# Optimization experiments

Measured on AMD Instinct MI355X. Metric: run time of the kernel, lower is better.

Reference implementation:

```python
import jax, jax.numpy as jnp
import numpy as np

N, IN_SZ, OUT_SZ = 8192, 512, 64

def setup_inputs() -> dict:
    key = jax.random.key(0)
    ks = jax.random.split(key, 7)
    s_in = 1.0 / np.sqrt(IN_SZ)
    inp = {
        "input": jax.random.normal(ks[0], (N, IN_SZ), dtype=jnp.float32),
        "Wq": jax.random.uniform(ks[1], (OUT_SZ, IN_SZ), jnp.float32, -s_in, s_in),
        "bq": jax.random.uniform(ks[2], (OUT_SZ,), jnp.float32, -s_in, s_in),
        "Wk": jax.random.uniform(ks[3], (OUT_SZ, IN_SZ), jnp.float32, -s_in, s_in),
        "bk": jax.random.uniform(ks[4], (OUT_SZ,), jnp.float32, -s_in, s_in),
        "Wv": jax.random.uniform(ks[5], (OUT_SZ, IN_SZ), jnp.float32, -s_in, s_in),
        "bv": jax.random.uniform(ks[6], (OUT_SZ,), jnp.float32, -s_in, s_in),
    }
    return inp

def reference(input, Wq, bq, Wk, bk, Wv, bv):
    # torch nn.Linear: x @ W.T + b
    q = input @ Wq.T + bq  # [N, out]
    k = input @ Wk.T + bk  # [N, out]
    v = input @ Wv.T + bv  # [N, out]
    # NOTE: original module has NO 1/sqrt(d) scaling.
    scores = jax.nn.softmax(q @ k.T, axis=-1)  # [N, N]
    return scores @ v  # [N, out]
```

## Files before the change

kernel.cpp:

```cpp
#include <hip/hip_runtime.h>
#include <math.h>

#define SA_N   8192
#define SA_IN  512
#define SA_D   64
#define G_SPL  16

typedef short s16x8 __attribute__((ext_vector_type(8)));
typedef float f32x16 __attribute__((ext_vector_type(16)));

#define MFMA32(A, B, C) __builtin_amdgcn_mfma_f32_32x32x16_bf16((A), (B), (C), 0, 0, 0)

static __device__ __forceinline__ unsigned short f2bf_rn(float x) {
    unsigned int u = __float_as_uint(x);
    unsigned int r = (u + 0x7FFFu + ((u >> 16) & 1u)) >> 16;
    return (unsigned short)r;
}

static __device__ __forceinline__ void trunc_split(float f, unsigned short* hi, unsigned short* lo) {
    unsigned int u = __float_as_uint(f);
    *hi = (unsigned short)(u >> 16);
    float lf = f - __uint_as_float(u & 0xFFFF0000u);
    *lo = (unsigned short)(__float_as_uint(lf) >> 16);
}

static __device__ __forceinline__ void split8(const float4 a, const float4 b, s16x8* xh, s16x8* xl) {
    union { unsigned int u[4]; s16x8 v; } H, L;
    const float f[8] = {a.x, a.y, a.z, a.w, b.x, b.y, b.z, b.w};
#pragma unroll
    for (int p = 0; p < 4; ++p) {
        const unsigned int u0 = __float_as_uint(f[2 * p]);
        const unsigned int u1 = __float_as_uint(f[2 * p + 1]);
        H.u[p] = (u0 >> 16) | (u1 & 0xFFFF0000u);
        const float l0 = f[2 * p]     - __uint_as_float(u0 & 0xFFFF0000u);
        const float l1 = f[2 * p + 1] - __uint_as_float(u1 & 0xFFFF0000u);
        L.u[p] = (__float_as_uint(l0) >> 16) | (__float_as_uint(l1) & 0xFFFF0000u);
    }
    *xh = H.v; *xl = L.v;
}

static __device__ __forceinline__ s16x8 pack_rn8(const float4 a, const float4 b) {
    union { unsigned int u[4]; s16x8 v; } P;
    const float f[8] = {a.x, a.y, a.z, a.w, b.x, b.y, b.z, b.w};
#pragma unroll
    for (int p = 0; p < 4; ++p)
        P.u[p] = (unsigned int)f2bf_rn(f[2 * p]) | ((unsigned int)f2bf_rn(f[2 * p + 1]) << 16);
    return P.v;
}

__global__ __launch_bounds__(256, 2) void qkv_kernel(
    const float* __restrict__ in,
    const float* __restrict__ Wq, const float* __restrict__ bq,
    const float* __restrict__ Wk, const float* __restrict__ bk,
    const float* __restrict__ Wv, const float* __restrict__ bv,
    unsigned short* __restrict__ Qhi, unsigned short* __restrict__ Qlo,
    unsigned short* __restrict__ KhiF, unsigned short* __restrict__ KloF,
    unsigned short* __restrict__ VF)
{
    __shared__ float cbuf[2][4][64][20];
    __shared__ __align__(16) unsigned short stage[4096];
    const int t    = threadIdx.x;
    const int w    = t >> 6;
    const int lane = t & 63;
    const int h    = lane >> 5;
    const int q32  = lane & 31;
    const int mat  = blockIdx.x >> 8;
    const int jt   = blockIdx.x & 255;
    const int rows0 = jt * 32;

    const float* W = (mat == 0) ? Wq : (mat == 1 ? Wk : Wv);
    const float* B = (mat == 0) ? bq : (mat == 1 ? bk : bv);

    f32x16 accA[2] = {};
    f32x16 accB[2] = {};

#pragma unroll 2
    for (int ksl = 0; ksl < 8; ++ksl) {
        const int ks = (w << 3) + ksl;
        const float* xp = in + (size_t)(rows0 + q32) * SA_IN + ks * 16 + h * 8;
        const float4 xa = *(const float4*)xp;
        const float4 xb = *(const float4*)(xp + 4);
        s16x8 xh, xl;
        split8(xa, xb, &xh, &xl);
#pragma unroll
        for (int mt = 0; mt < 2; ++mt) {
            const float* wp = W + (size_t)(mt * 32 + q32) * SA_IN + ks * 16 + h * 8;
            const float4 wa = *(const float4*)wp;
            const float4 wb = *(const float4*)(wp + 4);
            if (mat < 2) {
                s16x8 ah, al;
                split8(wa, wb, &ah, &al);
                accA[mt] = MFMA32(ah, xh, accA[mt]);
                accB[mt] = MFMA32(ah, xl, accB[mt]);
                accA[mt] = MFMA32(al, xh, accA[mt]);
            } else {
                const s16x8 ah = pack_rn8(wa, wb);
                accA[mt] = MFMA32(ah, xh, accA[mt]);
            }
        }
    }

#pragma unroll
    for (int mt = 0; mt < 2; ++mt) {
        f32x16 tot = accA[mt];
        if (mat < 2) {
#pragma unroll
            for (int r = 0; r < 16; ++r) tot[r] += accB[mt][r];
        }
#pragma unroll
        for (int rg = 0; rg < 4; ++rg) {
            float4 vv = { tot[4 * rg + 0], tot[4 * rg + 1],
                          tot[4 * rg + 2], tot[4 * rg + 3] };
            *(float4*)&cbuf[mt][w][lane][4 * rg] = vv;
        }
    }
    __syncthreads();
    if (w < 2) {
        const int mt = w;
        float c[16];
#pragma unroll
        for (int rg = 0; rg < 4; ++rg) {
            const float4 s0 = *(const float4*)&cbuf[mt][0][lane][4 * rg];
            const float4 s1 = *(const float4*)&cbuf[mt][1][lane][4 * rg];
            const float4 s2 = *(const float4*)&cbuf[mt][2][lane][4 * rg];
            const float4 s3 = *(const float4*)&cbuf[mt][3][lane][4 * rg];
            c[4 * rg + 0] = (s0.x + s1.x) + (s2.x + s3.x);
            c[4 * rg + 1] = (s0.y + s1.y) + (s2.y + s3.y);
            c[4 * rg + 2] = (s0.z + s1.z) + (s2.z + s3.z);
            c[4 * rg + 3] = (s0.w + s1.w) + (s2.w + s3.w);
        }
#pragma unroll
        for (int r = 0; r < 16; ++r) {
            const int o = mt * 32 + (r & 3) + 8 * (r >> 2) + 4 * h;
            const float val = c[r] + B[o];
            if (mat == 0) {
                unsigned short hi, lo;
                trunc_split(val, &hi, &lo);
                stage[q32 * 64 + o]        = hi;
                stage[2048 + q32 * 64 + o] = lo;
            } else if (mat == 1) {
                unsigned short hi, lo;
                trunc_split(val, &hi, &lo);
                const int kl_ = ((o >> 4) * 64 + ((o >> 3) & 1) * 32 + q32) * 8 + (o & 7);
                stage[kl_]        = hi;
                stage[2048 + kl_] = lo;
            } else {
                const int vl_ = ((o >> 5) * 2 + ((q32 >> 4) & 1)) * 512
                              + ((q32 >> 3) & 1) * 256 + (o & 31) * 8 + (q32 & 7);
                stage[vl_] = f2bf_rn(val);
            }
        }
    }
    __syncthreads();

    {
        const uint4* st4 = (const uint4*)stage;
        if (mat == 0) {
            for (int i = t; i < 512; i += 256) {
                unsigned short* dst = ((i < 256) ? Qhi : Qlo) + (size_t)rows0 * 64 + (i & 255) * 8;
                *(uint4*)dst = st4[i];
            }
        } else if (mat == 1) {
            for (int i = t; i < 512; i += 256) {
                unsigned short* dst = ((i < 256) ? KhiF : KloF) + (size_t)jt * 2048 + (i & 255) * 8;
                *(uint4*)dst = st4[i];
            }
        } else {
            *(uint4*)(VF + (size_t)jt * 2048 + t * 8) = st4[t];
        }
    }
}

__global__ __launch_bounds__(256, 2) void attn_kernel(
    const unsigned short* __restrict__ Qhi, const unsigned short* __restrict__ Qlo,
    const unsigned short* __restrict__ KhiF, const unsigned short* __restrict__ KloF,
    const unsigned short* __restrict__ VF,
    unsigned short* __restrict__ Opart, float* __restrict__ Lpart)
{
    const int t    = threadIdx.x;
    const int w    = t >> 6;
    const int lane = t & 63;
    const int h    = lane >> 5;
    const int q32  = lane & 31;
    const int qb   = blockIdx.x >> 4;
    const int g    = blockIdx.x & 15;
    const int q0   = (qb * 4 + w) * 32;

    s16x8 qh[4], ql[4];
#pragma unroll
    for (int s = 0; s < 4; ++s) {
        const size_t off = (size_t)(q0 + q32) * 64 + s * 16 + h * 8;
        qh[s] = *reinterpret_cast<const s16x8*>(Qhi + off);
        ql[s] = *reinterpret_cast<const s16x8*>(Qlo + off);
    }

    const s16x8* KH = reinterpret_cast<const s16x8*>(KhiF);
    const s16x8* KL = reinterpret_cast<const s16x8*>(KloF);
    const s16x8* VV = reinterpret_cast<const s16x8*>(VF);

    f32x16 O0 = {}, O1 = {};
    float lsum = 0.f;

    auto process = [&](const s16x8* kh, const s16x8* kl, const s16x8* vv) {
        f32x16 Sa = {}, Sb = {}, Sc = {};
#pragma unroll
        for (int s = 0; s < 4; ++s) {
            Sa = MFMA32(kh[s], qh[s], Sa);
            Sb = MFMA32(kh[s], ql[s], Sb);
            Sc = MFMA32(kl[s], qh[s], Sc);
        }

        float e[16];
#pragma unroll
        for (int r = 0; r < 16; ++r) e[r] = __expf((Sa[r] + Sb[r]) + Sc[r]);
        lsum += (((e[0] + e[1]) + (e[2] + e[3])) + ((e[4] + e[5]) + (e[6] + e[7])))
              + (((e[8] + e[9]) + (e[10] + e[11])) + ((e[12] + e[13]) + (e[14] + e[15])));

        unsigned int pk[8];
#pragma unroll
        for (int j2 = 0; j2 < 8; ++j2)
            pk[j2] = (__float_as_uint(e[2 * j2]) >> 16) | (__float_as_uint(e[2 * j2 + 1]) & 0xFFFF0000u);

        unsigned int x[8];
#pragma unroll
        for (int j2 = 0; j2 < 8; ++j2) x[j2] = (unsigned int)__shfl_xor((int)pk[j2], 32, 64);

        union { unsigned int u[4]; s16x8 v; } P0, P1;
        P0.u[0] = h ? x[2]  : pk[0];
        P0.u[1] = h ? x[3]  : pk[1];
        P0.u[2] = h ? pk[2] : x[0];
        P0.u[3] = h ? pk[3] : x[1];
        P1.u[0] = h ? x[6]  : pk[4];
        P1.u[1] = h ? x[7]  : pk[5];
        P1.u[2] = h ? pk[6] : x[4];
        P1.u[3] = h ? pk[7] : x[5];

        O0 = MFMA32(vv[0], P0.v, O0);
        O0 = MFMA32(vv[1], P1.v, O0);
        O1 = MFMA32(vv[2], P0.v, O1);
        O1 = MFMA32(vv[3], P1.v, O1);
    };

    for (int it = 0; it < 16; it += 2) {
        const int jtA = g * 16 + it;
        const int jtB = jtA + 1;
        s16x8 khA[4], klA[4], vA[4], khB[4], klB[4], vB[4];
#pragma unroll
        for (int s = 0; s < 4; ++s) {
            khA[s] = KH[(jtA * 4 + s) * 64 + lane];
            klA[s] = KL[(jtA * 4 + s) * 64 + lane];
            vA[s]  = VV[(jtA * 4 + s) * 64 + lane];
            khB[s] = KH[(jtB * 4 + s) * 64 + lane];
            klB[s] = KL[(jtB * 4 + s) * 64 + lane];
            vB[s]  = VV[(jtB * 4 + s) * 64 + lane];
        }
        process(khA, klA, vA);
        process(khB, klB, vB);
    }

    lsum += __shfl_xor(lsum, 32, 64);

    const size_t qg = (size_t)g * SA_N + q0 + q32;
#pragma unroll
    for (int rg = 0; rg < 4; ++rg) {
        const int d0 = 8 * rg + 4 * h;
        uint2 s0, s1;
        s0.x = (unsigned int)f2bf_rn(O0[4 * rg + 0]) | ((unsigned int)f2bf_rn(O0[4 * rg + 1]) << 16);
        s0.y = (unsigned int)f2bf_rn(O0[4 * rg + 2]) | ((unsigned int)f2bf_rn(O0[4 * rg + 3]) << 16);
        s1.x = (unsigned int)f2bf_rn(O1[4 * rg + 0]) | ((unsigned int)f2bf_rn(O1[4 * rg + 1]) << 16);
        s1.y = (unsigned int)f2bf_rn(O1[4 * rg + 2]) | ((unsigned int)f2bf_rn(O1[4 * rg + 3]) << 16);
        *(uint2*)(Opart + qg * 64 + d0)      = s0;
        *(uint2*)(Opart + qg * 64 + d0 + 32) = s1;
    }
    if (h == 0) Lpart[qg] = lsum;
}

__global__ __launch_bounds__(256) void combine_kernel(
    const unsigned short* __restrict__ Opart, const float* __restrict__ Lpart,
    float* __restrict__ out)
{
    const int tid = blockIdx.x * 256 + threadIdx.x;
    const int q  = tid >> 5;
    const int dp = tid & 31;
    const unsigned int* OP = (const unsigned int*)Opart;
    float s0 = 0.f, s1 = 0.f, lt = 0.f;
#pragma unroll
    for (int g = 0; g < G_SPL; ++g) {
        const unsigned int v = OP[((size_t)g * SA_N + q) * 32 + dp];
        s0 += __uint_as_float(v << 16);
        s1 += __uint_as_float(v & 0xFFFF0000u);
        lt += Lpart[(size_t)g * SA_N + q];
    }
    float2 r = { s0 / lt, s1 / lt };
    *(float2*)&out[(size_t)q * 64 + dp * 2] = r;
}

extern "C" void kernel_launch(void* const* d_in, const int* in_sizes, int n_in,
                              void* d_out, int out_size, void* d_ws, size_t ws_size,
                              hipStream_t stream) {
    const float* input = (const float*)d_in[0];
    const float* Wq    = (const float*)d_in[1];
    const float* bq    = (const float*)d_in[2];
    const float* Wk    = (const float*)d_in[3];
    const float* bk    = (const float*)d_in[4];
    const float* Wv    = (const float*)d_in[5];
    const float* bv    = (const float*)d_in[6];
    float* out = (float*)d_out;

    const size_t SEG = (size_t)SA_N * 64;
    unsigned short* Qhi  = (unsigned short*)d_ws;
    unsigned short* Qlo  = Qhi  + SEG;
    unsigned short* KhiF = Qlo  + SEG;
    unsigned short* KloF = KhiF + SEG;
    unsigned short* VF   = KloF + SEG;
    unsigned short* Opart = VF  + SEG;
    float*          Lpart = (float*)(Opart + (size_t)G_SPL * SA_N * 64);

    qkv_kernel<<<768, 256, 0, stream>>>(input, Wq, bq, Wk, bk, Wv, bv,
                                        Qhi, Qlo, KhiF, KloF, VF);
    attn_kernel<<<64 * G_SPL, 256, 0, stream>>>(Qhi, Qlo, KhiF, KloF, VF, Opart, Lpart);
    combine_kernel<<<1024, 256, 0, stream>>>(Opart, Lpart, out);
}
```

Measured before the change: 146.9 us.

## Stage K/V tiles through double-buffered LDS and use exp2 with prescaled Q

The attention kernel now cooperatively loads each K-hi, K-lo and V tile into a double-buffered shared-memory buffer, prefetching the next tile into registers while computing the current one. This replaces the earlier scheme where each of the four waves loaded the same tiles from global memory. Q is prescaled by log2(e) in the projection kernel so the softmax can use the hardware exp2, and the three split-precision score MFMAs now accumulate into a single register. Packing uses a byte-permute instruction. The cost is a block-wide barrier per tile and less instruction-level parallelism from the single accumulator chain.

```diff
diff --git a/kernel.cpp b/kernel.cpp
--- a/kernel.cpp
+++ b/kernel.cpp
@@ -5,6 +5,7 @@
 #define SA_IN  512
 #define SA_D   64
 #define G_SPL  16
+#define LOG2E  1.44269504f
 
 typedef short s16x8 __attribute__((ext_vector_type(8)));
 typedef float f32x16 __attribute__((ext_vector_type(16)));
@@ -24,6 +25,10 @@
     *lo = (unsigned short)(__float_as_uint(lf) >> 16);
 }
 
+static __device__ __forceinline__ unsigned int pack_hi16(unsigned int u0, unsigned int u1) {
+    return __builtin_amdgcn_perm(u1, u0, 0x07060302u);
+}
+
 static __device__ __forceinline__ void split8(const float4 a, const float4 b, s16x8* xh, s16x8* xl) {
     union { unsigned int u[4]; s16x8 v; } H, L;
     const float f[8] = {a.x, a.y, a.z, a.w, b.x, b.y, b.z, b.w};
@@ -31,10 +36,10 @@
     for (int p = 0; p < 4; ++p) {
         const unsigned int u0 = __float_as_uint(f[2 * p]);
         const unsigned int u1 = __float_as_uint(f[2 * p + 1]);
-        H.u[p] = (u0 >> 16) | (u1 & 0xFFFF0000u);
+        H.u[p] = pack_hi16(u0, u1);
         const float l0 = f[2 * p]     - __uint_as_float(u0 & 0xFFFF0000u);
         const float l1 = f[2 * p + 1] - __uint_as_float(u1 & 0xFFFF0000u);
-        L.u[p] = (__float_as_uint(l0) >> 16) | (__float_as_uint(l1) & 0xFFFF0000u);
+        L.u[p] = pack_hi16(__float_as_uint(l0), __float_as_uint(l1));
     }
     *xh = H.v; *xl = L.v;
 }
@@ -132,8 +137,9 @@
 #pragma unroll
         for (int r = 0; r < 16; ++r) {
             const int o = mt * 32 + (r & 3) + 8 * (r >> 2) + 4 * h;
-            const float val = c[r] + B[o];
+            float val = c[r] + B[o];
             if (mat == 0) {
+                val *= LOG2E;
                 unsigned short hi, lo;
                 trunc_split(val, &hi, &lo);
                 stage[q32 * 64 + o]        = hi;
@@ -177,6 +183,7 @@
     const unsigned short* __restrict__ VF,
     unsigned short* __restrict__ Opart, float* __restrict__ Lpart)
 {
+    __shared__ __align__(16) unsigned short kbuf[2][3][2048];
     const int t    = threadIdx.x;
     const int w    = t >> 6;
     const int lane = t & 63;
@@ -185,6 +192,7 @@
     const int qb   = blockIdx.x >> 4;
     const int g    = blockIdx.x & 15;
     const int q0   = (qb * 4 + w) * 32;
+    const int jt0  = g * 16;
 
     s16x8 qh[4], ql[4];
 #pragma unroll
@@ -194,32 +202,57 @@
         ql[s] = *reinterpret_cast<const s16x8*>(Qlo + off);
     }
 
-    const s16x8* KH = reinterpret_cast<const s16x8*>(KhiF);
-    const s16x8* KL = reinterpret_cast<const s16x8*>(KloF);
-    const s16x8* VV = reinterpret_cast<const s16x8*>(VF);
+    {
+        const size_t base = (size_t)jt0 * 2048 + t * 8;
+        const uint4 a = *(const uint4*)(KhiF + base);
+        const uint4 b = *(const uint4*)(KloF + base);
+        const uint4 c = *(const uint4*)(VF  + base);
+        *(uint4*)&kbuf[0][0][t * 8] = a;
+        *(uint4*)&kbuf[0][1][t * 8] = b;
+        *(uint4*)&kbuf[0][2][t * 8] = c;
+    }
+    __syncthreads();
 
     f32x16 O0 = {}, O1 = {};
     float lsum = 0.f;
 
-    auto process = [&](const s16x8* kh, const s16x8* kl, const s16x8* vv) {
-        f32x16 Sa = {}, Sb = {}, Sc = {};
+    for (int it = 0; it < 16; ++it) {
+        const int p = it & 1;
+
+        uint4 na, nb, nc;
+        if (it < 15) {
+            const size_t base = (size_t)(jt0 + it + 1) * 2048 + t * 8;
+            na = *(const uint4*)(KhiF + base);
+            nb = *(const uint4*)(KloF + base);
+            nc = *(const uint4*)(VF  + base);
+        }
+
+        s16x8 kh[4], kl[4], vv[4];
 #pragma unroll
         for (int s = 0; s < 4; ++s) {
-            Sa = MFMA32(kh[s], qh[s], Sa);
-            Sb = MFMA32(kh[s], ql[s], Sb);
-            Sc = MFMA32(kl[s], qh[s], Sc);
-        }
+            kh[s] = *(const s16x8*)&kbuf[p][0][(s * 64 + lane) * 8];
+            kl[s] = *(const s16x8*)&kbuf[p][1][(s * 64 + lane) * 8];
+            vv[s] = *(const s16x8*)&kbuf[p][2][(s * 64 + lane) * 8];
+        }
+
+        f32x16 S = {};
+#pragma unroll
+        for (int s = 0; s < 4; ++s) S = MFMA32(kh[s], qh[s], S);
+#pragma unroll
+        for (int s = 0; s < 4; ++s) S = MFMA32(kh[s], ql[s], S);
+#pragma unroll
+        for (int s = 0; s < 4; ++s) S = MFMA32(kl[s], qh[s], S);
 
         float e[16];
 #pragma unroll
-        for (int r = 0; r < 16; ++r) e[r] = __expf((Sa[r] + Sb[r]) + Sc[r]);
+        for (int r = 0; r < 16; ++r) e[r] = __builtin_amdgcn_exp2f(S[r]);
         lsum += (((e[0] + e[1]) + (e[2] + e[3])) + ((e[4] + e[5]) + (e[6] + e[7])))
               + (((e[8] + e[9]) + (e[10] + e[11])) + ((e[12] + e[13]) + (e[14] + e[15])));
 
         unsigned int pk[8];
 #pragma unroll
         for (int j2 = 0; j2 < 8; ++j2)
-            pk[j2] = (__float_as_uint(e[2 * j2]) >> 16) | (__float_as_uint(e[2 * j2 + 1]) & 0xFFFF0000u);
+            pk[j2] = pack_hi16(__float_as_uint(e[2 * j2]), __float_as_uint(e[2 * j2 + 1]));
 
         unsigned int x[8];
 #pragma unroll
@@ -239,23 +272,13 @@
         O0 = MFMA32(vv[1], P1.v, O0);
         O1 = MFMA32(vv[2], P0.v, O1);
         O1 = MFMA32(vv[3], P1.v, O1);
-    };
-
-    for (int it = 0; it < 16; it += 2) {
-        const int jtA = g * 16 + it;
-        const int jtB = jtA + 1;
-        s16x8 khA[4], klA[4], vA[4], khB[4], klB[4], vB[4];
-#pragma unroll
-        for (int s = 0; s < 4; ++s) {
-            khA[s] = KH[(jtA * 4 + s) * 64 + lane];
-            klA[s] = KL[(jtA * 4 + s) * 64 + lane];
-            vA[s]  = VV[(jtA * 4 + s) * 64 + lane];
-            khB[s] = KH[(jtB * 4 + s) * 64 + lane];
-            klB[s] = KL[(jtB * 4 + s) * 64 + lane];
-            vB[s]  = VV[(jtB * 4 + s) * 64 + lane];
-        }
-        process(khA, klA, vA);
-        process(khB, klB, vB);
+
+        if (it < 15) {
+            *(uint4*)&kbuf[1 - p][0][t * 8] = na;
+            *(uint4*)&kbuf[1 - p][1][t * 8] = nb;
+            *(uint4*)&kbuf[1 - p][2][t * 8] = nc;
+        }
+        __syncthreads();
     }
 
     lsum += __shfl_xor(lsum, 32, 64);
```

Result: faster. 135.2 us (-8.0%).
